# Kernel tuning notes

Measured on AMD Instinct MI355X. Metric: run time of the kernel, lower is better.

Reference implementation:

```python
import math
import jax, jax.numpy as jnp
import numpy as np

DIM = 1024
HEADS = 16
HEAD_DIM = DIM // HEADS
NEG = -10000.0


def setup_inputs() -> dict:
    key = jax.random.key(0)
    ks = jax.random.split(key, 9)
    B, S = 2, 2048
    s = 1.0 / math.sqrt(DIM)
    inp = {
        "x": jax.random.normal(ks[0], (B, S, DIM), dtype=jnp.float32),
        "Wq": jax.random.normal(ks[1], (DIM, DIM), dtype=jnp.float32) * s,
        "bq": jnp.zeros((DIM,), dtype=jnp.float32),
        "Wk": jax.random.normal(ks[2], (DIM, DIM), dtype=jnp.float32) * s,
        "bk": jnp.zeros((DIM,), dtype=jnp.float32),
        "Wv": jax.random.normal(ks[3], (DIM, DIM), dtype=jnp.float32) * s,
        "bv": jnp.zeros((DIM,), dtype=jnp.float32),
        "Wo": jax.random.normal(ks[4], (DIM, DIM), dtype=jnp.float32) * s,
        "bo": jnp.zeros((DIM,), dtype=jnp.float32),
    }
    return inp


def reference(x, Wq, bq, Wk, bk, Wv, bv, Wo, bo):
    B, S, D = x.shape
    q = x @ Wq + bq
    k = x @ Wk + bk
    v = x @ Wv + bv
    # [B, H, S, hd]
    def split_heads(t):
        return t.reshape(B, S, HEADS, HEAD_DIM).transpose(0, 2, 1, 3)
    q, k, v = split_heads(q), split_heads(k), split_heads(v)
    scores = jnp.einsum("bhqd,bhkd->bhqk", q, k) / math.sqrt(HEAD_DIM)
    causal = jnp.tril(jnp.ones((S, S), dtype=bool))  # [S, S]
    scores = jnp.where(causal[None, None], scores, NEG)
    probs = jax.nn.softmax(scores, axis=-1)
    ctx = jnp.einsum("bhqk,bhkd->bhqd", probs, v)  # [B, H, S, hd]
    ctx = ctx.transpose(0, 2, 1, 3).reshape(B, S, D)
    out = ctx @ Wo + bo
    return out
```

## Files before the change

kernel.cpp:

```cpp
#include <hip/hip_runtime.h>
#include <hip/hip_bf16.h>
#include <math.h>

#define DIMX 1024
#define HEADSX 16
#define HDX 64
#define BBX 2
#define SSX 2048
#define MMX (BBX*SSX)

typedef __bf16 bf16x8 __attribute__((ext_vector_type(8)));
typedef __bf16 bf16x4 __attribute__((ext_vector_type(4)));
typedef float  f32x4  __attribute__((ext_vector_type(4)));

#define NEGF (-1e30f)

static __device__ __forceinline__ void gload16(const void* g, void* l) {
  __builtin_amdgcn_global_load_lds(
      (const __attribute__((address_space(1))) unsigned int*)g,
      (__attribute__((address_space(3))) unsigned int*)l, 16, 0, 0);
}

__global__ __launch_bounds__(256) void k_convert_x(const float* __restrict__ x,
                                                   __bf16* __restrict__ xb) {
  int i = (blockIdx.x * 256 + threadIdx.x) * 4;
  float4 v = *(const float4*)&x[i];
  bf16x4 o = { (__bf16)v.x, (__bf16)v.y, (__bf16)v.z, (__bf16)v.w };
  *(bf16x4*)&xb[i] = o;
}

__global__ __launch_bounds__(256) void k_transpose_w(
    const float* __restrict__ Wq, const float* __restrict__ Wk,
    const float* __restrict__ Wv, const float* __restrict__ Wo,
    __bf16* __restrict__ wqkvT, __bf16* __restrict__ woT) {
  __shared__ __bf16 tile[64][65];
  const int mat = blockIdx.y;
  const float* src = (mat == 0) ? Wq : (mat == 1) ? Wk : (mat == 2) ? Wv : Wo;
  __bf16* dst = (mat < 3) ? (wqkvT + (size_t)mat * DIMX * DIMX) : woT;
  const int tx = blockIdx.x & 15, ty = blockIdx.x >> 4;
  const int k0 = ty * 64, n0 = tx * 64;
  #pragma unroll
  for (int rep = 0; rep < 16; ++rep) {
    int idx = rep * 256 + threadIdx.x;
    int r = idx >> 6, c = idx & 63;
    tile[r][c] = (__bf16)src[(size_t)(k0 + r) * DIMX + n0 + c];
  }
  __syncthreads();
  #pragma unroll
  for (int rep = 0; rep < 16; ++rep) {
    int idx = rep * 256 + threadIdx.x;
    int r = idx >> 6, c = idx & 63;
    dst[(size_t)(n0 + r) * DIMX + k0 + c] = tile[c][r];
  }
}

template<int EPI>
__global__ __launch_bounds__(256) void k_gemm(
    const __bf16* __restrict__ A,
    const __bf16* __restrict__ Bt,
    const float* __restrict__ b0, const float* __restrict__ b1,
    const float* __restrict__ b2,
    __bf16* __restrict__ qb, __bf16* __restrict__ kb, __bf16* __restrict__ vtb,
    float* __restrict__ outf) {
  constexpr int BK = 32, K = 1024;
  __shared__ __bf16 As[128 * BK];
  __shared__ __bf16 Bs[128 * BK];
  const int tid = threadIdx.x, lane = tid & 63, wave = tid >> 6;
  const int g = lane >> 4, r16 = lane & 15;
  const int wm = wave & 1, wn = wave >> 1;
  const int m0 = blockIdx.x * 128, n0 = blockIdx.y * 128;

  f32x4 acc[4][4] = {};

  for (int k0 = 0; k0 < K; k0 += BK) {
    __syncthreads();
    #pragma unroll
    for (int i = 0; i < 2; ++i) {
      int c = wave * 64 + lane + 256 * i;
      gload16(&A [(size_t)(m0 + (c >> 2)) * K + k0 + (c & 3) * 8],
              (char*)As + (size_t)(wave * 64 + 256 * i) * 16);
      gload16(&Bt[(size_t)(n0 + (c >> 2)) * K + k0 + (c & 3) * 8],
              (char*)Bs + (size_t)(wave * 64 + 256 * i) * 16);
    }
    __syncthreads();
    bf16x8 af[4], bfr[4];
    #pragma unroll
    for (int i = 0; i < 4; ++i)
      af[i]  = *(const bf16x8*)&As[(wm * 64 + i * 16 + r16) * BK + g * 8];
    #pragma unroll
    for (int j = 0; j < 4; ++j)
      bfr[j] = *(const bf16x8*)&Bs[(wn * 64 + j * 16 + r16) * BK + g * 8];
    #pragma unroll
    for (int i = 0; i < 4; ++i)
      #pragma unroll
      for (int j = 0; j < 4; ++j)
        acc[i][j] = __builtin_amdgcn_mfma_f32_16x16x32_bf16(af[i], bfr[j],
                                                            acc[i][j], 0, 0, 0);
  }

  #pragma unroll
  for (int i = 0; i < 4; ++i) {
    #pragma unroll
    for (int j = 0; j < 4; ++j) {
      #pragma unroll
      for (int r = 0; r < 4; ++r) {
        int m = m0 + wm * 64 + i * 16 + 4 * g + r;
        int n = n0 + wn * 64 + j * 16 + r16;
        float v = acc[i][j][r];
        if constexpr (EPI == 0) {
          int proj = n >> 10, w = n & 1023, h = w >> 6, d = w & 63;
          const float* bp = (proj == 0) ? b0 : (proj == 1) ? b1 : b2;
          v += bp[w];
          int b = m >> 11, s = m & 2047, bh = b * HEADSX + h;
          if (proj == 0)      qb [((size_t)bh * SSX + s) * HDX + d] = (__bf16)v;
          else if (proj == 1) kb [((size_t)bh * SSX + s) * HDX + d] = (__bf16)v;
          else                vtb[((size_t)bh * HDX + d) * SSX + s] = (__bf16)v;
        } else {
          outf[(size_t)m * DIMX + n] = v + b0[n];
        }
      }
    }
  }
}

__global__ __launch_bounds__(256, 4) void k_attn(
    const __bf16* __restrict__ qb, const __bf16* __restrict__ kb,
    const __bf16* __restrict__ vtb, __bf16* __restrict__ ctxb) {
  const int tid = threadIdx.x;
  const int lane = tid & 63, wq = tid >> 6;
  const int g = lane >> 4, r16 = lane & 15;
  const int bh = blockIdx.y;
  const int qx = (blockIdx.x + bh) & 31;
  const int q0 = qx * 64 + wq * 16;
  const int b = bh >> 4, h = bh & 15;

  const __bf16* Q  = qb  + (size_t)bh * SSX * HDX;
  const __bf16* Kp = kb  + (size_t)bh * SSX * HDX;
  const __bf16* Vt = vtb + (size_t)bh * HDX * SSX;

  __shared__ __bf16 Ks[2][64 * 64];
  __shared__ __bf16 Vs[2][64 * 64];
  __shared__ unsigned Pld[4][512];

  bf16x8 qf[2];
  qf[0] = *(const bf16x8*)&Q[(size_t)(q0 + r16) * HDX + g * 8];
  qf[1] = *(const bf16x8*)&Q[(size_t)(q0 + r16) * HDX + 32 + g * 8];

  f32x4 acc[4] = {};
  float mrun = NEGF, lrun = 0.f;
  const int qrow = q0 + r16;

  const int ntiles = qx + 1;
  const float scale2 = 0.18033688011112042f;

  auto STAGE = [&](int buf, int t) {
    const int kv0 = t * 64;
    #pragma unroll
    for (int i = 0; i < 2; ++i) {
      int c = tid + 256 * i;
      int r = c >> 3;
      int cb = (c & 7) ^ (r & 7);
      gload16(&Kp[(size_t)(kv0 + r) * HDX + cb * 8],
              (char*)Ks[buf] + (size_t)(wq * 64 + 256 * i) * 16);
      gload16(&Vt[(size_t)r * SSX + kv0 + cb * 8],
              (char*)Vs[buf] + (size_t)(wq * 64 + 256 * i) * 16);
    }
  };

  STAGE(0, 0);
  __syncthreads();

  for (int t = 0; t < ntiles; ++t) {
    const int cur = t & 1;
    if (t + 1 < ntiles) STAGE(cur ^ 1, t + 1);
    const int kv0 = t * 64;

    f32x4 sac[4] = {};
    #pragma unroll
    for (int kk = 0; kk < 2; ++kk)
      #pragma unroll
      for (int jj = 0; jj < 4; ++jj) {
        int rr = jj * 16 + r16;
        bf16x8 kf = *(const bf16x8*)
            &Ks[cur][rr * 64 + (((kk << 2) + g) ^ (rr & 7)) * 8];
        sac[jj] = __builtin_amdgcn_mfma_f32_16x16x32_bf16(kf, qf[kk], sac[jj],
                                                          0, 0, 0);
      }

    float pv[4][4];
    float mt = NEGF;
    const bool last = (t == ntiles - 1);
    #pragma unroll
    for (int jj = 0; jj < 4; ++jj)
      #pragma unroll
      for (int r = 0; r < 4; ++r) {
        float s = sac[jj][r] * scale2;
        if (last) {
          int kcol = kv0 + jj * 16 + 4 * g + r;
          s = (kcol > qrow) ? NEGF : s;
        }
        pv[jj][r] = s;
        mt = fmaxf(mt, s);
      }
    mt = fmaxf(mt, __shfl_xor(mt, 16));
    mt = fmaxf(mt, __shfl_xor(mt, 32));

    float mnew = fmaxf(mrun, mt);
    float fac = exp2f(mrun - mnew);
    mrun = mnew;

    float rs = 0.f;
    #pragma unroll
    for (int jj = 0; jj < 4; ++jj)
      #pragma unroll
      for (int r = 0; r < 4; ++r) {
        float p = exp2f(pv[jj][r] - mrun);
        pv[jj][r] = p;
        rs += p;
      }
    lrun = lrun * fac + rs;
    #pragma unroll
    for (int j2 = 0; j2 < 4; ++j2)
      #pragma unroll
      for (int r = 0; r < 4; ++r)
        acc[j2][r] *= fac;

    #pragma unroll
    for (int jj = 0; jj < 4; ++jj)
      #pragma unroll
      for (int rp = 0; rp < 2; ++rp) {
        unsigned w;
        asm("v_cvt_pk_bf16_f32 %0, %1, %2"
            : "=v"(w) : "v"(pv[jj][2 * rp]), "v"(pv[jj][2 * rp + 1]));
        int c = jj * 8 + g * 2 + rp;
        int addr = r16 * 32 + (((c >> 2) ^ (r16 & 7)) << 2) + (c & 3);
        Pld[wq][addr] = w;
      }

    bf16x8 pf[2];
    #pragma unroll
    for (int half = 0; half < 2; ++half) {
      int c = half * 16 + g * 4;
      int addr = r16 * 32 + (((c >> 2) ^ (r16 & 7)) << 2);
      pf[half] = *(const bf16x8*)&Pld[wq][addr];
    }
    #pragma unroll
    for (int j2 = 0; j2 < 4; ++j2)
      #pragma unroll
      for (int half = 0; half < 2; ++half) {
        int dd = j2 * 16 + r16;
        bf16x8 vf = *(const bf16x8*)
            &Vs[cur][dd * 64 + (((half << 2) + g) ^ (dd & 7)) * 8];
        acc[j2] = __builtin_amdgcn_mfma_f32_16x16x32_bf16(vf, pf[half],
                                                          acc[j2], 0, 0, 0);
      }
    __syncthreads();
  }

  lrun += __shfl_xor(lrun, 16);
  lrun += __shfl_xor(lrun, 32);
  const float inv = 1.f / lrun;

  const int s = q0 + r16;
  #pragma unroll
  for (int j2 = 0; j2 < 4; ++j2)
    #pragma unroll
    for (int r = 0; r < 4; ++r) {
      int d = j2 * 16 + 4 * g + r;
      ctxb[((size_t)(b * SSX + s)) * DIMX + h * HDX + d] =
          (__bf16)(acc[j2][r] * inv);
    }
}

extern "C" void kernel_launch(void* const* d_in, const int* in_sizes, int n_in,
                              void* d_out, int out_size, void* d_ws,
                              size_t ws_size, hipStream_t stream) {
  const float* x  = (const float*)d_in[0];
  const float* Wq = (const float*)d_in[1];
  const float* bq = (const float*)d_in[2];
  const float* Wk = (const float*)d_in[3];
  const float* bk = (const float*)d_in[4];
  const float* Wv = (const float*)d_in[5];
  const float* bv = (const float*)d_in[6];
  const float* Wo = (const float*)d_in[7];
  const float* bo = (const float*)d_in[8];
  float* out = (float*)d_out;

  char* ws = (char*)d_ws;
  __bf16* xb    = (__bf16*)(ws);
  __bf16* wqkvT = (__bf16*)(ws + ((size_t)8  << 20));
  __bf16* woT   = (__bf16*)(ws + ((size_t)14 << 20));
  __bf16* qb    = (__bf16*)(ws + ((size_t)16 << 20));
  __bf16* kb    = (__bf16*)(ws + ((size_t)24 << 20));
  __bf16* vtb   = (__bf16*)(ws + ((size_t)32 << 20));
  __bf16* ctxb  = xb;

  k_convert_x<<<4096, 256, 0, stream>>>(x, xb);
  k_transpose_w<<<dim3(256, 4), 256, 0, stream>>>(Wq, Wk, Wv, Wo, wqkvT, woT);
  k_gemm<0><<<dim3(32, 24), 256, 0, stream>>>(xb, wqkvT, bq, bk, bv,
                                              qb, kb, vtb, nullptr);
  k_attn<<<dim3(32, 32), 256, 0, stream>>>(qb, kb, vtb, ctxb);
  k_gemm<1><<<dim3(32, 8), 256, 0, stream>>>(ctxb, woT, bo, nullptr, nullptr,
                                             nullptr, nullptr, nullptr, out);
}
```

Baseline: 134.0 us.

## Pair low and high causal query tiles per block with XCD-aware head mapping

Each attention block now handles two query tiles, p and 31-p, so every block does the same total number of KV tiles under the causal mask. Each staged K/V tile is shared between the two tiles, which also reduces K/V loads. Blocks are mapped to heads so that the blocks of one head land on the same XCD for L2 locality. MFMA sections are wrapped with s_setprio to favour matrix issue. The grid halves to 512 blocks and launch bounds drop to 2 waves per SIMD to fit the doubled register state, which lowers occupancy.

After: 121.9 us. 9.1% less time.

```diff
diff --git a/kernel.cpp b/kernel.cpp
--- a/kernel.cpp
+++ b/kernel.cpp
@@ -123,16 +123,22 @@
   }
 }
 
-__global__ __launch_bounds__(256, 4) void k_attn(
+__global__ __launch_bounds__(256, 2) void k_attn(
     const __bf16* __restrict__ qb, const __bf16* __restrict__ kb,
     const __bf16* __restrict__ vtb, __bf16* __restrict__ ctxb) {
   const int tid = threadIdx.x;
   const int lane = tid & 63, wq = tid >> 6;
   const int g = lane >> 4, r16 = lane & 15;
-  const int bh = blockIdx.y;
-  const int qx = (blockIdx.x + bh) & 31;
-  const int q0 = qx * 64 + wq * 16;
+
+  const int id = blockIdx.x;
+  const int xcd = id & 7, idx = id >> 3;
+  const int bh = xcd * 4 + (idx & 3);
+  const int p  = idx >> 2;
   const int b = bh >> 4, h = bh & 15;
+
+  const int ntL = p + 1, ntH = 32 - p;
+  const int q0L = p * 64 + wq * 16;
+  const int q0H = (31 - p) * 64 + wq * 16;
 
   const __bf16* Q  = qb  + (size_t)bh * SSX * HDX;
   const __bf16* Kp = kb  + (size_t)bh * SSX * HDX;
@@ -142,15 +148,16 @@
   __shared__ __bf16 Vs[2][64 * 64];
   __shared__ unsigned Pld[4][512];
 
-  bf16x8 qf[2];
-  qf[0] = *(const bf16x8*)&Q[(size_t)(q0 + r16) * HDX + g * 8];
-  qf[1] = *(const bf16x8*)&Q[(size_t)(q0 + r16) * HDX + 32 + g * 8];
-
-  f32x4 acc[4] = {};
-  float mrun = NEGF, lrun = 0.f;
-  const int qrow = q0 + r16;
-
-  const int ntiles = qx + 1;
+  bf16x8 qfL[2], qfH[2];
+  qfL[0] = *(const bf16x8*)&Q[(size_t)(q0L + r16) * HDX + g * 8];
+  qfL[1] = *(const bf16x8*)&Q[(size_t)(q0L + r16) * HDX + 32 + g * 8];
+  qfH[0] = *(const bf16x8*)&Q[(size_t)(q0H + r16) * HDX + g * 8];
+  qfH[1] = *(const bf16x8*)&Q[(size_t)(q0H + r16) * HDX + 32 + g * 8];
+
+  f32x4 accL[4] = {}, accH[4] = {};
+  float mrunL = NEGF, lrunL = 0.f;
+  float mrunH = NEGF, lrunH = 0.f;
+
   const float scale2 = 0.18033688011112042f;
 
   auto STAGE = [&](int buf, int t) {
@@ -167,15 +174,10 @@
     }
   };
 
-  STAGE(0, 0);
-  __syncthreads();
-
-  for (int t = 0; t < ntiles; ++t) {
-    const int cur = t & 1;
-    if (t + 1 < ntiles) STAGE(cur ^ 1, t + 1);
-    const int kv0 = t * 64;
-
+  auto SUBTILE = [&](const bf16x8* qf, f32x4* acc, float& mrun, float& lrun,
+                     int qrow, bool last, int kv0, int cur) {
     f32x4 sac[4] = {};
+    __builtin_amdgcn_s_setprio(1);
     #pragma unroll
     for (int kk = 0; kk < 2; ++kk)
       #pragma unroll
@@ -186,10 +188,10 @@
         sac[jj] = __builtin_amdgcn_mfma_f32_16x16x32_bf16(kf, qf[kk], sac[jj],
                                                           0, 0, 0);
       }
+    __builtin_amdgcn_s_setprio(0);
 
     float pv[4][4];
     float mt = NEGF;
-    const bool last = (t == ntiles - 1);
     #pragma unroll
     for (int jj = 0; jj < 4; ++jj)
       #pragma unroll
@@ -214,9 +216,9 @@
     for (int jj = 0; jj < 4; ++jj)
       #pragma unroll
       for (int r = 0; r < 4; ++r) {
-        float p = exp2f(pv[jj][r] - mrun);
-        pv[jj][r] = p;
-        rs += p;
+        float px = exp2f(pv[jj][r] - mrun);
+        pv[jj][r] = px;
+        rs += px;
       }
     lrun = lrun * fac + rs;
     #pragma unroll
@@ -244,6 +246,7 @@
       int addr = r16 * 32 + (((c >> 2) ^ (r16 & 7)) << 2);
       pf[half] = *(const bf16x8*)&Pld[wq][addr];
     }
+    __builtin_amdgcn_s_setprio(1);
     #pragma unroll
     for (int j2 = 0; j2 < 4; ++j2)
       #pragma unroll
@@ -254,22 +257,40 @@
         acc[j2] = __builtin_amdgcn_mfma_f32_16x16x32_bf16(vf, pf[half],
                                                           acc[j2], 0, 0, 0);
       }
+    __builtin_amdgcn_s_setprio(0);
+  };
+
+  STAGE(0, 0);
+  __syncthreads();
+
+  for (int t = 0; t < ntH; ++t) {
+    const int cur = t & 1;
+    if (t + 1 < ntH) STAGE(cur ^ 1, t + 1);
+    const int kv0 = t * 64;
+
+    SUBTILE(qfH, accH, mrunH, lrunH, q0H + r16, t == ntH - 1, kv0, cur);
+    if (t < ntL)
+      SUBTILE(qfL, accL, mrunL, lrunL, q0L + r16, t == ntL - 1, kv0, cur);
+
     __syncthreads();
   }
 
-  lrun += __shfl_xor(lrun, 16);
-  lrun += __shfl_xor(lrun, 32);
-  const float inv = 1.f / lrun;
-
-  const int s = q0 + r16;
-  #pragma unroll
-  for (int j2 = 0; j2 < 4; ++j2)
-    #pragma unroll
-    for (int r = 0; r < 4; ++r) {
-      int d = j2 * 16 + 4 * g + r;
-      ctxb[((size_t)(b * SSX + s)) * DIMX + h * HDX + d] =
-          (__bf16)(acc[j2][r] * inv);
-    }
+  auto EPIL = [&](f32x4* acc, float lrun, int q0) {
+    lrun += __shfl_xor(lrun, 16);
+    lrun += __shfl_xor(lrun, 32);
+    const float inv = 1.f / lrun;
+    const int s = q0 + r16;
+    #pragma unroll
+    for (int j2 = 0; j2 < 4; ++j2)
+      #pragma unroll
+      for (int r = 0; r < 4; ++r) {
+        int d = j2 * 16 + 4 * g + r;
+        ctxb[((size_t)(b * SSX + s)) * DIMX + h * HDX + d] =
+            (__bf16)(acc[j2][r] * inv);
+      }
+  };
+  EPIL(accH, lrunH, q0H);
+  EPIL(accL, lrunL, q0L);
 }
 
 extern "C" void kernel_launch(void* const* d_in, const int* in_sizes, int n_in,
@@ -299,7 +320,7 @@
   k_transpose_w<<<dim3(256, 4), 256, 0, stream>>>(Wq, Wk, Wv, Wo, wqkvT, woT);
   k_gemm<0><<<dim3(32, 24), 256, 0, stream>>>(xb, wqkvT, bq, bk, bv,
                                               qb, kb, vtb, nullptr);
-  k_attn<<<dim3(32, 32), 256, 0, stream>>>(qb, kb, vtb, ctxb);
+  k_attn<<<512, 256, 0, stream>>>(qb, kb, vtb, ctxb);
   k_gemm<1><<<dim3(32, 8), 256, 0, stream>>>(ctxb, woT, bo, nullptr, nullptr,
                                              nullptr, nullptr, nullptr, out);
 }
```
